# Optimization experiments

Measured on AMD Instinct MI355X. Metric: run time of the kernel, lower is better.

## Reference

```python
import jax, jax.numpy as jnp
import numpy as np
import math

DIMS = 2560
N_HEADS = 32
ROT_DIM = 32  # partial rotary (Phi-2)
BASE = 10000.0
B, L = 1, 2048


def apply_rope(x, rot_dim=ROT_DIM, base=BASE, offset=0):
    # x: [B, H, L, hd]; rotate first rot_dim features, pass rest through
    Lx = x.shape[2]
    D = rot_dim // 2
    pos = jnp.arange(offset, offset + Lx, dtype=jnp.float32)              # [L]
    freq = jnp.exp(-jnp.arange(D, dtype=jnp.float32) * (math.log(base) / D))  # [D]
    theta = pos[:, None] * freq[None, :]                                   # [L, D]
    cos, sin = jnp.cos(theta), jnp.sin(theta)
    x1 = x[..., :D]
    x2 = x[..., D:rot_dim]
    rx1 = x1 * cos - x2 * sin
    rx2 = x1 * sin + x2 * cos
    return jnp.concatenate([rx1, rx2, x[..., rot_dim:]], axis=-1)


def setup_inputs() -> dict:
    key = jax.random.key(0)
    k1, k2, k3, k4, k5 = jax.random.split(key, 5)
    x = jax.random.normal(k1, (B, L, DIMS), dtype=jnp.float32)
    Wqkv_w = jax.random.normal(k2, (3 * DIMS, DIMS), dtype=jnp.float32) * 0.02
    Wqkv_b = jax.random.normal(k3, (3 * DIMS,), dtype=jnp.float32) * 0.02
    out_w = jax.random.normal(k4, (DIMS, DIMS), dtype=jnp.float32) * 0.02
    out_b = jax.random.normal(k5, (DIMS,), dtype=jnp.float32) * 0.02
    # additive causal mask, broadcast over batch/heads
    mask = jnp.triu(jnp.full((L, L), -1e9, dtype=jnp.float32), k=1)[None, None]
    return {"x": x, "Wqkv_w": Wqkv_w, "Wqkv_b": Wqkv_b,
            "out_w": out_w, "out_b": out_b, "mask": mask}


def reference(x, Wqkv_w, Wqkv_b, out_w, out_b, mask):
    Bx, Lx, _ = x.shape
    hd = DIMS // N_HEADS  # 80
    qkv = x @ Wqkv_w.T + Wqkv_b                          # [B, L, 3*dims]
    q, k, v = jnp.split(qkv, 3, axis=-1)
    def to_heads(t):
        return t.reshape(Bx, Lx, N_HEADS, hd).transpose(0, 2, 1, 3)  # [B,H,L,hd]
    q, k, v = to_heads(q), to_heads(k), to_heads(v)
    q = apply_rope(q)
    k = apply_rope(k)
    scale = 1.0 / math.sqrt(hd)
    scores = scale * jnp.einsum('bhqd,bhkd->bhqk', q, k) + mask  # [B,H,L,L]
    probs = jax.nn.softmax(scores, axis=-1)
    out = jnp.einsum('bhqk,bhkd->bhqd', probs, v)
    out = out.transpose(0, 2, 1, 3).reshape(Bx, Lx, DIMS)
    return out @ out_w.T + out_b
```

## Files before the change

### kernel.cpp

```cpp
#include <hip/hip_runtime.h>
#include <cstdint>
#include <cmath>

typedef __attribute__((ext_vector_type(4))) float f32x4;
typedef __attribute__((ext_vector_type(8))) short s16x8;

#define LOG2E 1.4426950408889634f

__device__ __forceinline__ unsigned short f2bf(float f) {
    unsigned int u = __float_as_uint(f);
    u += 0x7FFFu + ((u >> 16) & 1u);
    return (unsigned short)(u >> 16);
}
__device__ __forceinline__ float bf2f(unsigned short s) {
    return __uint_as_float(((unsigned int)s) << 16);
}

__device__ __forceinline__ void async_copy16(const void* g, void* l) {
    __builtin_amdgcn_global_load_lds(
        (const __attribute__((address_space(1))) unsigned int*)(uintptr_t)g,
        (__attribute__((address_space(3))) unsigned int*)(uintptr_t)l,
        16, 0, 0);
}

__global__ __launch_bounds__(256) void cast_bf16_kernel(const float* __restrict__ in,
                                                        unsigned short* __restrict__ out,
                                                        int n4) {
    int i = blockIdx.x * 256 + threadIdx.x;
    if (i < n4) {
        float4 v = ((const float4*)in)[i];
        ushort4 o;
        o.x = f2bf(v.x); o.y = f2bf(v.y); o.z = f2bf(v.z); o.w = f2bf(v.w);
        ((ushort4*)out)[i] = o;
    }
}

template <bool BF16_OUT>
__global__ __launch_bounds__(256) void gemm_bt(const unsigned short* __restrict__ A,
                                               const unsigned short* __restrict__ B,
                                               const float* __restrict__ bias,
                                               void* __restrict__ Cout,
                                               int M, int N, int K) {
    __shared__ unsigned short As[128 * 64];
    __shared__ unsigned short Bs[128 * 64];
    const int tid  = threadIdx.x;
    const int lane = tid & 63;
    const int wv   = tid >> 6;
    const int m0 = blockIdx.y * 128;
    const int n0 = blockIdx.x * 128;
    const int w_row = (wv >> 1) * 64;
    const int w_col = (wv & 1) * 64;
    const int fr = lane & 15;
    const int fg = lane >> 4;
    const int srow = lane >> 3;
    const int scol = ((lane & 7) ^ srow) * 8;
    const int rofs0 = ((fg ^ (fr & 7))) * 8;
    const int rofs1 = rofs0 ^ 32;

    f32x4 acc[4][4];
    const f32x4 zf = {0.f, 0.f, 0.f, 0.f};
    for (int r = 0; r < 4; ++r)
        for (int c = 0; c < 4; ++c) acc[r][c] = zf;

    const unsigned short* gA = A + (size_t)(m0 + wv * 32 + srow) * K + scol;
    const unsigned short* gB = B + (size_t)(n0 + wv * 32 + srow) * K + scol;

    for (int k0 = 0; k0 < K; k0 += 64) {
        for (int i = 0; i < 4; ++i)
            async_copy16(gA + (size_t)i * 8 * K + k0, &As[(wv * 32 + i * 8) * 64]);
        for (int i = 0; i < 4; ++i)
            async_copy16(gB + (size_t)i * 8 * K + k0, &Bs[(wv * 32 + i * 8) * 64]);
        __syncthreads();
        {
            s16x8 af[4], bf[4];
            for (int r = 0; r < 4; ++r)
                af[r] = *(const s16x8*)&As[(w_row + r * 16 + fr) * 64 + rofs0];
            for (int c = 0; c < 4; ++c)
                bf[c] = *(const s16x8*)&Bs[(w_col + c * 16 + fr) * 64 + rofs0];
            for (int r = 0; r < 4; ++r)
                for (int c = 0; c < 4; ++c)
                    acc[r][c] = __builtin_amdgcn_mfma_f32_16x16x32_bf16(af[r], bf[c], acc[r][c], 0, 0, 0);
        }
        {
            s16x8 af[4], bf[4];
            for (int r = 0; r < 4; ++r)
                af[r] = *(const s16x8*)&As[(w_row + r * 16 + fr) * 64 + rofs1];
            for (int c = 0; c < 4; ++c)
                bf[c] = *(const s16x8*)&Bs[(w_col + c * 16 + fr) * 64 + rofs1];
            for (int r = 0; r < 4; ++r)
                for (int c = 0; c < 4; ++c)
                    acc[r][c] = __builtin_amdgcn_mfma_f32_16x16x32_bf16(af[r], bf[c], acc[r][c], 0, 0, 0);
        }
        __syncthreads();
    }

    const int rb = (lane >> 4) * 4;
    for (int c = 0; c < 4; ++c) {
        int col = n0 + w_col + c * 16 + fr;
        float bv = bias[col];
        for (int r = 0; r < 4; ++r) {
            int row = m0 + w_row + r * 16 + rb;
            for (int q = 0; q < 4; ++q) {
                float v = acc[r][c][q] + bv;
                if constexpr (BF16_OUT)
                    ((unsigned short*)Cout)[(size_t)(row + q) * N + col] = f2bf(v);
                else
                    ((float*)Cout)[(size_t)(row + q) * N + col] = v;
            }
        }
    }
}


#define BAR()   __builtin_amdgcn_s_barrier()
#define VMW(N)  asm volatile("s_waitcnt vmcnt(" #N ")" ::: "memory")

#define STAGE2(gXb, XsBuf, rb, kk) \
    async_copy16(gXb + (size_t)(rb) * K + (kk), (void*)&XsBuf[(rb) * 64])

#define ST_AS0(b, kk) { STAGE2(gAb, As[b], rbA_0, kk);      STAGE2(gAb, As[b], rbA_1, kk); }
#define ST_AS1(b, kk) { STAGE2(gAb, As[b], rbA_0 + 64, kk); STAGE2(gAb, As[b], rbA_1 + 64, kk); }
#define ST_BS0(b, kk) { STAGE2(gBb, Bs[b], rbB_0, kk);      STAGE2(gBb, Bs[b], rbB_1, kk); }
#define ST_BS1(b, kk) { STAGE2(gBb, Bs[b], rbB_0 + 32, kk); STAGE2(gBb, Bs[b], rbB_1 + 32, kk); }

#define READ_A(b, mh) \
    _Pragma("unroll") \
    for (int mm_ = 0; mm_ < 4; ++mm_) { \
        const unsigned short* ap_ = &As[b][(wr * 128 + (mh) * 64 + mm_ * 16 + fr) * 64]; \
        Ar[mm_][0] = *(const s16x8*)(ap_ + rofs0); \
        Ar[mm_][1] = *(const s16x8*)(ap_ + rofs1); \
    }

#define READ_B(b, nh, Brg) \
    _Pragma("unroll") \
    for (int nn_ = 0; nn_ < 2; ++nn_) { \
        const unsigned short* bp_ = &Bs[b][(wc * 64 + (nh) * 32 + nn_ * 16 + fr) * 64]; \
        Brg[nn_][0] = *(const s16x8*)(bp_ + rofs0); \
        Brg[nn_][1] = *(const s16x8*)(bp_ + rofs1); \
    }

#define MFMA_Q(mh, nh, Brg) \
    _Pragma("unroll") \
    for (int mm_ = 0; mm_ < 4; ++mm_) { \
        _Pragma("unroll") \
        for (int nn_ = 0; nn_ < 2; ++nn_) { \
            acc[(mh) * 4 + mm_][(nh) * 2 + nn_] = __builtin_amdgcn_mfma_f32_16x16x32_bf16( \
                Ar[mm_][0], Brg[nn_][0], acc[(mh) * 4 + mm_][(nh) * 2 + nn_], 0, 0, 0); \
            acc[(mh) * 4 + mm_][(nh) * 2 + nn_] = __builtin_amdgcn_mfma_f32_16x16x32_bf16( \
                Ar[mm_][1], Brg[nn_][1], acc[(mh) * 4 + mm_][(nh) * 2 + nn_], 0, 0, 0); \
        } \
    }

#define GROUP(b, t) { \
    int x1_ = (t) + 1; if (x1_ >= ktiles) x1_ -= ktiles; \
    int x2_ = (t) + 2; if (x2_ >= ktiles) x2_ -= ktiles; \
    const int kn1 = x1_ << 6; \
    const int kn2 = x2_ << 6; \
     \
    __builtin_amdgcn_s_setprio(1); MFMA_Q(0, 0, Br0); __builtin_amdgcn_s_setprio(0); \
    VMW(6); \
    READ_B(b, 1, Br1); \
    ST_AS1((b) ^ 1, kn1); \
    BAR(); \
     \
    __builtin_amdgcn_s_setprio(1); MFMA_Q(0, 1, Br1); __builtin_amdgcn_s_setprio(0); \
    VMW(6); \
    READ_A(b, 1); \
    ST_AS0(b, kn2); \
    BAR(); \
     \
    __builtin_amdgcn_s_setprio(1); MFMA_Q(1, 1, Br1); __builtin_amdgcn_s_setprio(0); \
    VMW(6); \
    ST_BS0(b, kn2); \
    BAR(); \
     \
    __builtin_amdgcn_s_setprio(1); MFMA_Q(1, 0, Br0); __builtin_amdgcn_s_setprio(0); \
    VMW(6); \
    READ_A((b) ^ 1, 0); \
    READ_B((b) ^ 1, 0, Br0); \
    ST_BS1(b, kn2); \
    BAR(); \
}

__global__ __launch_bounds__(512, 2) void gemm256_bt(const unsigned short* __restrict__ A,
                                                     const unsigned short* __restrict__ B,
                                                     const float* __restrict__ bias,
                                                     unsigned short* __restrict__ C,
                                                     int M, int N, int K) {
    __shared__ unsigned short As[2][256 * 64];
    __shared__ unsigned short Bs[2][256 * 64];
    const int tid  = threadIdx.x;
    const int lane = tid & 63;
    const int wv   = tid >> 6;
    const int wr   = wv >> 2;
    const int wc   = wv & 3;
    const int j     = blockIdx.x & 7;
    const int local = blockIdx.x >> 3;
    const int strip = 2 * (j & 3) + (local & 1);
    const int panel = (j >> 2) * 15 + (local >> 1);
    const int m0 = strip * 256;
    const int n0 = panel * 256;
    const int fr = lane & 15;
    const int fg = lane >> 4;
    const int rofs0 = (fg ^ (fr & 7)) * 8;
    const int rofs1 = rofs0 ^ 32;
    const int rlane = lane >> 3;
    const int swzc  = ((lane & 7) ^ (rlane & 7)) * 8;
    const int idx0 = wv * 2, idx1 = wv * 2 + 1;
    const int rbA_0 = idx0 * 8 + ((idx0 >= 8) ? 64 : 0);
    const int rbA_1 = idx1 * 8 + ((idx1 >= 8) ? 64 : 0);
    const int rbB_0 = (idx0 >> 2) * 64 + (idx0 & 3) * 8;
    const int rbB_1 = (idx1 >> 2) * 64 + (idx1 & 3) * 8;
    const int ktiles = K >> 6;

    const unsigned short* gAb = A + (size_t)(m0 + rlane) * K + swzc;
    const unsigned short* gBb = B + (size_t)(n0 + rlane) * K + swzc;

    f32x4 acc[8][4];
    const f32x4 zf = {0.f, 0.f, 0.f, 0.f};
#pragma unroll
    for (int i = 0; i < 8; ++i)
#pragma unroll
        for (int jj = 0; jj < 4; ++jj) acc[i][jj] = zf;

    s16x8 Ar[4][2], Br0[2][2], Br1[2][2];

    ST_AS0(0, 0); ST_AS1(0, 0); ST_BS0(0, 0); ST_BS1(0, 0);
    ST_AS0(1, 64); ST_BS0(1, 64); ST_BS1(1, 64);
    VMW(6);
    BAR();
    READ_A(0, 0);
    READ_B(0, 0, Br0);

    const int nit = ktiles >> 1;
    for (int it = 0; it < nit; ++it) {
        GROUP(0, it * 2);
        GROUP(1, it * 2 + 1);
    }

    const int rb = (lane >> 4) * 4;
#pragma unroll
    for (int nn = 0; nn < 4; ++nn) {
        int col = n0 + wc * 64 + nn * 16 + fr;
        float bv = bias[col];
#pragma unroll
        for (int mm = 0; mm < 8; ++mm) {
            int row = m0 + wr * 128 + mm * 16 + rb;
#pragma unroll
            for (int q = 0; q < 4; ++q) {
                float v = acc[mm][nn][q] + bv;
                C[(size_t)(row + q) * N + col] = f2bf(v);
            }
        }
    }
}

__global__ __launch_bounds__(256) void rope_q_kernel(unsigned short* __restrict__ qkv) {
    int g = blockIdx.x * 256 + threadIdx.x;
    int c = g & 1;
    int h = (g >> 1) & 31;
    int p = g >> 6;
    size_t base = (size_t)p * 7680 + h * 80 + c * 8;
    s16x8 x1v = *(const s16x8*)(qkv + base);
    s16x8 x2v = *(const s16x8*)(qkv + base + 16);
    s16x8 o1, o2;
    for (int j = 0; j < 8; ++j) {
        int dp = c * 8 + j;
        float freq = expf(-(float)dp * 0.57564627324851142f);
        float sn, cs;
        sincosf((float)p * freq, &sn, &cs);
        float x1 = bf2f((unsigned short)x1v[j]);
        float x2 = bf2f((unsigned short)x2v[j]);
        o1[j] = (short)f2bf(x1 * cs - x2 * sn);
        o2[j] = (short)f2bf(x1 * sn + x2 * cs);
    }
    *(s16x8*)(qkv + base)      = o1;
    *(s16x8*)(qkv + base + 16) = o2;
}

__global__ __launch_bounds__(256) void rope_pack_k_kernel(const unsigned short* __restrict__ qkv,
                                                          unsigned short* __restrict__ Kp) {
    int g = blockIdx.x * 256 + threadIdx.x;
    int c   = g % 12;
    int h   = (g / 12) & 31;
    int pos = g / 384;
    int d0 = c * 8;
    const unsigned short* kb = qkv + (size_t)pos * 7680 + 2560 + h * 80;
    s16x8 v = {0, 0, 0, 0, 0, 0, 0, 0};
    if (c >= 4) {
        if (d0 < 80) v = *(const s16x8*)(kb + d0);
    } else if (c < 2) {
        s16x8 x1v = *(const s16x8*)(kb + d0);
        s16x8 x2v = *(const s16x8*)(kb + d0 + 16);
        for (int j = 0; j < 8; ++j) {
            int dp = d0 + j;
            float freq = expf(-(float)dp * 0.57564627324851142f);
            float sn, cs;
            sincosf((float)pos * freq, &sn, &cs);
            v[j] = (short)f2bf(bf2f((unsigned short)x1v[j]) * cs -
                               bf2f((unsigned short)x2v[j]) * sn);
        }
    } else {
        s16x8 x1v = *(const s16x8*)(kb + d0 - 16);
        s16x8 x2v = *(const s16x8*)(kb + d0);
        for (int j = 0; j < 8; ++j) {
            int dp = d0 - 16 + j;
            float freq = expf(-(float)dp * 0.57564627324851142f);
            float sn, cs;
            sincosf((float)pos * freq, &sn, &cs);
            v[j] = (short)f2bf(bf2f((unsigned short)x1v[j]) * sn +
                               bf2f((unsigned short)x2v[j]) * cs);
        }
    }
    *(s16x8*)(Kp + ((size_t)h * 2048 + pos) * 96 + d0) = v;
}

__global__ __launch_bounds__(256) void pack_v_kernel(const unsigned short* __restrict__ qkv,
                                                     unsigned short* __restrict__ Vp) {
    int h  = blockIdx.x & 31;
    int g64 = blockIdx.x >> 5;
    int k0 = g64 * 64;
    int tid = threadIdx.x;
    for (int ci = tid; ci < 320; ci += 256) {
        int d   = ci % 80;
        int kbl = ci / 80;
        unsigned short tmp[16];
        for (int j = 0; j < 16; ++j)
            tmp[j] = qkv[(size_t)(k0 + kbl * 16 + j) * 7680 + 5120 + h * 80 + d];
        unsigned short* dst = Vp + ((size_t)h * 128 + g64 * 4 + kbl) * 1280 + d * 16;
        *(s16x8*)dst       = *(const s16x8*)&tmp[0];
        *(s16x8*)(dst + 8) = *(const s16x8*)&tmp[8];
    }
}

__global__ __launch_bounds__(256) void flash3_kernel(const unsigned short* __restrict__ qkv,
                                                     const unsigned short* __restrict__ Kp,
                                                     const unsigned short* __restrict__ Vp,
                                                     unsigned short* __restrict__ attn) {
    __shared__ unsigned short Pt[4][640];
    __shared__ float parts[2][16][84];
    __shared__ float parts_l[2][16];
    const int tid  = threadIdx.x;
    const int lane = tid & 63;
    const int wv   = tid >> 6;
    const int h = blockIdx.x & 31;
    const int p = blockIdx.x >> 5;
    const int s    = (wv < 2) ? p : (127 - p);
    const int j    = wv & 1;
    const int slot = wv >> 1;
    const int fr = lane & 15;
    const int fg = lane >> 4;
    const float k1 = 0.11180339887498949f * LOG2E;
    const int sm16 = s * 16;

    const int n    = s + 1;
    const int half = (n + 1) >> 1;
    const int kstart = (j ? half : 0) * 16;
    const int kend   = (j ? n : half) * 16;

    s16x8 qf[3];
    {
        const unsigned short* qb = qkv + (size_t)(sm16 + fr) * 7680 + h * 80;
        const s16x8 zs = {0, 0, 0, 0, 0, 0, 0, 0};
        for (int sd = 0; sd < 3; ++sd) {
            int d = 32 * sd + fg * 8;
            qf[sd] = (d < 80) ? *(const s16x8*)(qb + d) : zs;
        }
    }

    f32x4 O[5];
    const f32x4 zf = {0.f, 0.f, 0.f, 0.f};
    for (int t = 0; t < 5; ++t) O[t] = zf;
    float rs[4] = {0.f, 0.f, 0.f, 0.f};

    const unsigned short* kptr = Kp + (size_t)h * 2048 * 96 + (size_t)(kstart + fr) * 96 + fg * 8;
    const unsigned short* vptr = Vp + (size_t)h * 128 * 1280 + (size_t)(kstart >> 4) * 1280
                                 + (fg >> 1) * 1280 + fr * 16 + (fg & 1) * 8;
    unsigned short* Pw = &Pt[wv][0];

    for (int k0 = kstart; k0 < kend; k0 += 32) {
        s16x8 kb[2][3];
        for (int g = 0; g < 2; ++g)
            for (int sd = 0; sd < 3; ++sd)
                kb[g][sd] = *(const s16x8*)(kptr + g * 1536 + sd * 32);
        s16x8 vb[5];
        for (int t = 0; t < 5; ++t)
            vb[t] = *(const s16x8*)(vptr + t * 256);

        f32x4 sa[2] = {zf, zf};
        for (int g = 0; g < 2; ++g)
            for (int sd = 0; sd < 3; ++sd)
                sa[g] = __builtin_amdgcn_mfma_f32_16x16x32_bf16(qf[sd], kb[g][sd], sa[g], 0, 0, 0);

        if (k0 + 32 > sm16 || k0 + 32 > kend) {
            for (int g = 0; g < 2; ++g)
                for (int r = 0; r < 4; ++r) {
                    int key  = k0 + g * 16 + fr;
                    int qrow = sm16 + fg * 4 + r;
                    if (key > qrow || key >= kend) sa[g][r] = -1e30f;
                }
        }

        float pr[2][4];
        for (int g = 0; g < 2; ++g)
            for (int r = 0; r < 4; ++r)
                pr[g][r] = __builtin_amdgcn_exp2f(sa[g][r] * k1);
        for (int r = 0; r < 4; ++r) rs[r] += pr[0][r] + pr[1][r];
        for (int g = 0; g < 2; ++g)
            for (int r = 0; r < 4; ++r)
                Pw[(fg * 4 + r) * 40 + g * 16 + fr] =
                    (unsigned short)(__float_as_uint(pr[g][r]) >> 16);

        s16x8 pa = *(const s16x8*)(Pw + fr * 40 + fg * 8);
        for (int t = 0; t < 5; ++t)
            O[t] = __builtin_amdgcn_mfma_f32_16x16x32_bf16(pa, vb[t], O[t], 0, 0, 0);

        kptr += 3072;
        vptr += 2560;
    }

    for (int r = 0; r < 4; ++r) {
        float v = rs[r];
        v += __shfl_xor(v, 1);
        v += __shfl_xor(v, 2);
        v += __shfl_xor(v, 4);
        v += __shfl_xor(v, 8);
        rs[r] = v;
    }

    if (j) {
        for (int t = 0; t < 5; ++t)
            for (int r = 0; r < 4; ++r)
                parts[slot][fg * 4 + r][t * 16 + fr] = O[t][r];
        if (fr == 0)
            for (int r = 0; r < 4; ++r) parts_l[slot][fg * 4 + r] = rs[r];
    }
    __syncthreads();
    if (!j) {
        for (int r = 0; r < 4; ++r) {
            float rl = 1.0f / (rs[r] + parts_l[slot][fg * 4 + r]);
            int row = sm16 + fg * 4 + r;
            for (int t = 0; t < 5; ++t) {
                float v = (O[t][r] + parts[slot][fg * 4 + r][t * 16 + fr]) * rl;
                attn[(size_t)row * 2560 + h * 80 + t * 16 + fr] = f2bf(v);
            }
        }
    }
}

extern "C" void kernel_launch(void* const* d_in, const int* in_sizes, int n_in,
                              void* d_out, int out_size, void* d_ws, size_t ws_size,
                              hipStream_t stream) {
    const float* x    = (const float*)d_in[0];
    const float* wqkv = (const float*)d_in[1];
    const float* bqkv = (const float*)d_in[2];
    const float* outw = (const float*)d_in[3];
    const float* outb = (const float*)d_in[4];

    unsigned short* xb    = (unsigned short*)d_ws;
    unsigned short* wqkvb = xb + (size_t)2048 * 2560;
    unsigned short* Kp    = wqkvb;
    unsigned short* Vp    = wqkvb + (size_t)32 * 2048 * 96;
    unsigned short* outwb = wqkvb + (size_t)7680 * 2560;
    unsigned short* qkvb  = outwb + (size_t)2560 * 2560;
    unsigned short* attnb = qkvb  + (size_t)2048 * 7680;
    float* out = (float*)d_out;

    cast_bf16_kernel<<<2048 * 2560 / 4 / 256, 256, 0, stream>>>(x, xb, 2048 * 2560 / 4);
    cast_bf16_kernel<<<7680 * 2560 / 4 / 256, 256, 0, stream>>>(wqkv, wqkvb, 7680 * 2560 / 4);
    cast_bf16_kernel<<<2560 * 2560 / 4 / 256, 256, 0, stream>>>(outw, outwb, 2560 * 2560 / 4);

    gemm256_bt<<<240, 512, 0, stream>>>(xb, wqkvb, bqkv, qkvb, 2048, 7680, 2560);

    rope_q_kernel<<<2048 * 64 / 256, 256, 0, stream>>>(qkvb);
    rope_pack_k_kernel<<<2048 * 384 / 256, 256, 0, stream>>>(qkvb, Kp);
    pack_v_kernel<<<32 * 32, 256, 0, stream>>>(qkvb, Vp);

    flash3_kernel<<<2048, 256, 0, stream>>>(qkvb, Kp, Vp, attnb);

    gemm_bt<false><<<dim3(2560 / 128, 2048 / 128), 256, 0, stream>>>(
        attnb, outwb, outb, (void*)out, 2048, 2560, 2560);
}
```

Before: 414.1 us.

## Balance causal attention work evenly across four waves via unit-range splitting

Each block handles a short and a long query strip. Previously each strip went to two waves that split its keys in half, so the waves on the long strip carried most of the work. Now the combined 32-key units of both strips are divided evenly over all four waves. Partial O and row sums are merged through LDS atomicAdds, and a cooperative epilogue normalizes and writes both strips. The change also raises wave priority around the MFMA sections with s_setprio. The cost is shared-memory zeroing, atomic traffic and the reloading of Q per segment.

```diff
diff --git a/kernel.cpp b/kernel.cpp
--- a/kernel.cpp
+++ b/kernel.cpp
@@ -338,112 +338,134 @@
                                                      const unsigned short* __restrict__ Vp,
                                                      unsigned short* __restrict__ attn) {
     __shared__ unsigned short Pt[4][640];
-    __shared__ float parts[2][16][84];
+    __shared__ float parts_s[2][16][84];
     __shared__ float parts_l[2][16];
     const int tid  = threadIdx.x;
     const int lane = tid & 63;
     const int wv   = tid >> 6;
     const int h = blockIdx.x & 31;
     const int p = blockIdx.x >> 5;
-    const int s    = (wv < 2) ? p : (127 - p);
-    const int j    = wv & 1;
-    const int slot = wv >> 1;
     const int fr = lane & 15;
     const int fg = lane >> 4;
     const float k1 = 0.11180339887498949f * LOG2E;
-    const int sm16 = s * 16;
-
-    const int n    = s + 1;
-    const int half = (n + 1) >> 1;
-    const int kstart = (j ? half : 0) * 16;
-    const int kend   = (j ? n : half) * 16;
-
-    s16x8 qf[3];
-    {
-        const unsigned short* qb = qkv + (size_t)(sm16 + fr) * 7680 + h * 80;
-        const s16x8 zs = {0, 0, 0, 0, 0, 0, 0, 0};
-        for (int sd = 0; sd < 3; ++sd) {
-            int d = 32 * sd + fg * 8;
-            qf[sd] = (d < 80) ? *(const s16x8*)(qb + d) : zs;
-        }
-    }
+
+    for (int i = tid; i < 2 * 16 * 84; i += 256) ((float*)parts_s)[i] = 0.f;
+    if (tid < 32) ((float*)parts_l)[tid] = 0.f;
+    __syncthreads();
+
+    const int n1 = 128 - p;
+    const int U1 = (n1 + 1) >> 1;
+    const int U  = U1 + ((p + 2) >> 1);
+    const int lo = (wv * U) >> 2;
+    const int hi = ((wv + 1) * U) >> 2;
+    const int a1 = (lo < U1) ? lo : U1;
+    const int b1 = (hi < U1) ? hi : U1;
+    const int a0 = (lo > U1) ? (lo - U1) : 0;
+    const int b0 = (hi > U1) ? (hi - U1) : 0;
 
     f32x4 O[5];
     const f32x4 zf = {0.f, 0.f, 0.f, 0.f};
+    const s16x8 zs = {0, 0, 0, 0, 0, 0, 0, 0};
     for (int t = 0; t < 5; ++t) O[t] = zf;
     float rs[4] = {0.f, 0.f, 0.f, 0.f};
-
-    const unsigned short* kptr = Kp + (size_t)h * 2048 * 96 + (size_t)(kstart + fr) * 96 + fg * 8;
-    const unsigned short* vptr = Vp + (size_t)h * 128 * 1280 + (size_t)(kstart >> 4) * 1280
-                                 + (fg >> 1) * 1280 + fr * 16 + (fg & 1) * 8;
     unsigned short* Pw = &Pt[wv][0];
 
-    for (int k0 = kstart; k0 < kend; k0 += 32) {
-        s16x8 kb[2][3];
-        for (int g = 0; g < 2; ++g)
-            for (int sd = 0; sd < 3; ++sd)
-                kb[g][sd] = *(const s16x8*)(kptr + g * 1536 + sd * 32);
-        s16x8 vb[5];
-        for (int t = 0; t < 5; ++t)
-            vb[t] = *(const s16x8*)(vptr + t * 256);
-
-        f32x4 sa[2] = {zf, zf};
-        for (int g = 0; g < 2; ++g)
-            for (int sd = 0; sd < 3; ++sd)
-                sa[g] = __builtin_amdgcn_mfma_f32_16x16x32_bf16(qf[sd], kb[g][sd], sa[g], 0, 0, 0);
-
-        if (k0 + 32 > sm16 || k0 + 32 > kend) {
+    for (int seg = 0; seg < 2; ++seg) {
+        const int s_   = seg ? p : (127 - p);
+        const int slot = seg ? 0 : 1;
+        const int ua   = seg ? a0 : a1;
+        const int ub   = seg ? b0 : b1;
+        if (ua >= ub) continue;
+        const int sm16 = s_ * 16;
+        const int kend = sm16 + 16;
+
+        s16x8 qf[3];
+        {
+            const unsigned short* qb = qkv + (size_t)(sm16 + fr) * 7680 + h * 80;
+            for (int sd = 0; sd < 3; ++sd) {
+                int d = 32 * sd + fg * 8;
+                qf[sd] = (d < 80) ? *(const s16x8*)(qb + d) : zs;
+            }
+        }
+        const unsigned short* kptr = Kp + (size_t)h * 2048 * 96 + (size_t)(ua * 32 + fr) * 96 + fg * 8;
+        const unsigned short* vptr = Vp + (size_t)h * 128 * 1280 + (size_t)(ua * 2) * 1280
+                                     + (fg >> 1) * 1280 + fr * 16 + (fg & 1) * 8;
+
+        for (int u = ua; u < ub; ++u) {
+            const int k0 = u * 32;
+            s16x8 kb[2][3];
             for (int g = 0; g < 2; ++g)
-                for (int r = 0; r < 4; ++r) {
-                    int key  = k0 + g * 16 + fr;
-                    int qrow = sm16 + fg * 4 + r;
-                    if (key > qrow || key >= kend) sa[g][r] = -1e30f;
-                }
-        }
-
-        float pr[2][4];
-        for (int g = 0; g < 2; ++g)
+                for (int sd = 0; sd < 3; ++sd)
+                    kb[g][sd] = *(const s16x8*)(kptr + g * 1536 + sd * 32);
+            s16x8 vb[5];
+            for (int t = 0; t < 5; ++t)
+                vb[t] = *(const s16x8*)(vptr + t * 256);
+
+            f32x4 sa[2] = {zf, zf};
+            __builtin_amdgcn_s_setprio(1);
+            for (int g = 0; g < 2; ++g)
+                for (int sd = 0; sd < 3; ++sd)
+                    sa[g] = __builtin_amdgcn_mfma_f32_16x16x32_bf16(qf[sd], kb[g][sd], sa[g], 0, 0, 0);
+            __builtin_amdgcn_s_setprio(0);
+
+            if (k0 + 32 > sm16 || k0 + 32 > kend) {
+                for (int g = 0; g < 2; ++g)
+                    for (int r = 0; r < 4; ++r) {
+                        int key  = k0 + g * 16 + fr;
+                        int qrow = sm16 + fg * 4 + r;
+                        if (key > qrow || key >= kend) sa[g][r] = -1e30f;
+                    }
+            }
+            float pr[2][4];
+            for (int g = 0; g < 2; ++g)
+                for (int r = 0; r < 4; ++r)
+                    pr[g][r] = __builtin_amdgcn_exp2f(sa[g][r] * k1);
+            for (int r = 0; r < 4; ++r) rs[r] += pr[0][r] + pr[1][r];
+            for (int g = 0; g < 2; ++g)
+                for (int r = 0; r < 4; ++r)
+                    Pw[(fg * 4 + r) * 40 + g * 16 + fr] =
+                        (unsigned short)(__float_as_uint(pr[g][r]) >> 16);
+
+            s16x8 pa = *(const s16x8*)(Pw + fr * 40 + fg * 8);
+            __builtin_amdgcn_s_setprio(1);
+            for (int t = 0; t < 5; ++t)
+                O[t] = __builtin_amdgcn_mfma_f32_16x16x32_bf16(pa, vb[t], O[t], 0, 0, 0);
+            __builtin_amdgcn_s_setprio(0);
+
+            kptr += 3072;
+            vptr += 2560;
+        }
+
+        for (int r = 0; r < 4; ++r) {
+            float v = rs[r];
+            v += __shfl_xor(v, 1);
+            v += __shfl_xor(v, 2);
+            v += __shfl_xor(v, 4);
+            v += __shfl_xor(v, 8);
+            rs[r] = v;
+        }
+        if (fr == 0)
             for (int r = 0; r < 4; ++r)
-                pr[g][r] = __builtin_amdgcn_exp2f(sa[g][r] * k1);
-        for (int r = 0; r < 4; ++r) rs[r] += pr[0][r] + pr[1][r];
-        for (int g = 0; g < 2; ++g)
-            for (int r = 0; r < 4; ++r)
-                Pw[(fg * 4 + r) * 40 + g * 16 + fr] =
-                    (unsigned short)(__float_as_uint(pr[g][r]) >> 16);
-
-        s16x8 pa = *(const s16x8*)(Pw + fr * 40 + fg * 8);
-        for (int t = 0; t < 5; ++t)
-            O[t] = __builtin_amdgcn_mfma_f32_16x16x32_bf16(pa, vb[t], O[t], 0, 0, 0);
-
-        kptr += 3072;
-        vptr += 2560;
-    }
-
-    for (int r = 0; r < 4; ++r) {
-        float v = rs[r];
-        v += __shfl_xor(v, 1);
-        v += __shfl_xor(v, 2);
-        v += __shfl_xor(v, 4);
-        v += __shfl_xor(v, 8);
-        rs[r] = v;
-    }
-
-    if (j) {
+                atomicAdd(&parts_l[slot][fg * 4 + r], rs[r]);
         for (int t = 0; t < 5; ++t)
             for (int r = 0; r < 4; ++r)
-                parts[slot][fg * 4 + r][t * 16 + fr] = O[t][r];
-        if (fr == 0)
-            for (int r = 0; r < 4; ++r) parts_l[slot][fg * 4 + r] = rs[r];
-    }
+                atomicAdd(&parts_s[slot][fg * 4 + r][t * 16 + fr], O[t][r]);
+        for (int t = 0; t < 5; ++t) O[t] = zf;
+        for (int r = 0; r < 4; ++r) rs[r] = 0.f;
+    }
+
     __syncthreads();
-    if (!j) {
-        for (int r = 0; r < 4; ++r) {
-            float rl = 1.0f / (rs[r] + parts_l[slot][fg * 4 + r]);
-            int row = sm16 + fg * 4 + r;
-            for (int t = 0; t < 5; ++t) {
-                float v = (O[t][r] + parts[slot][fg * 4 + r][t * 16 + fr]) * rl;
-                attn[(size_t)row * 2560 + h * 80 + t * 16 + fr] = f2bf(v);
-            }
+    {
+        const int ri    = wv * 8 + (lane >> 3);
+        const int strip = ri >> 4;
+        const int row16 = ri & 15;
+        const int grow  = (strip ? (127 - p) : p) * 16 + row16;
+        const float rl  = 1.0f / parts_l[strip][row16];
+        const int c0 = lane & 7;
+        for (int i = 0; i < 10; ++i) {
+            int col = c0 + 8 * i;
+            float v = parts_s[strip][row16][col] * rl;
+            attn[(size_t)grow * 2560 + h * 80 + col] = f2bf(v);
         }
     }
 }
```

After: 447.0 us. 7.9% more time.
